# Optimization experiments

Hardware: AMD Instinct MI355X
Metric: run time of the kernel (lower is better)

Reference implementation:

```python
import jax, jax.numpy as jnp
import numpy as np

B, S, ENC, DEC, ATTN = 64, 2048, 512, 512, 256

def setup_inputs() -> dict:
    key = jax.random.key(0)
    k1, k2, k3, k4, k5 = jax.random.split(key, 5)
    s = 0.05
    return {
        "enc_outputs": jax.random.normal(k1, (B, S, ENC), dtype=jnp.float32),
        "dec_state": jax.random.normal(k2, (B, DEC), dtype=jnp.float32),
        "W_enc": jax.random.normal(k3, (ENC, ATTN), dtype=jnp.float32) * s,
        "W_dec": jax.random.normal(k4, (DEC, ATTN), dtype=jnp.float32) * s,
        "v": jax.random.normal(k5, (ATTN,), dtype=jnp.float32) * s,
    }

def reference(enc_outputs, dec_state, W_enc, W_dec, v):
    # enc_proj: [B,S,A], dec_proj: [B,1,A]
    enc_proj = jnp.einsum('bse,ea->bsa', enc_outputs, W_enc)
    dec_proj = jnp.einsum('bd,da->ba', dec_state, W_dec)[:, None, :]
    scores = jnp.einsum('bsa,a->bs', jnp.tanh(enc_proj + dec_proj), v)  # [B,S]
    attn_weights = jax.nn.softmax(scores, axis=-1)
    context = jnp.einsum('bs,bse->be', attn_weights, enc_outputs)  # [B,ENC]
    return (context, attn_weights)
```

## Files before the change

kernel.cpp:

```cpp
#include <hip/hip_runtime.h>
#include <hip/hip_bf16.h>
#include <stdint.h>

#define B_    64
#define S_    2048
#define ENC_  512
#define ATTN_ 256

typedef __bf16 bf16;
typedef bf16  bf16x8 __attribute__((ext_vector_type(8)));
typedef float f32x4  __attribute__((ext_vector_type(4)));

__device__ __forceinline__ float fexp2(float x) {
#if __has_builtin(__builtin_amdgcn_exp2f)
    return __builtin_amdgcn_exp2f(x);
#else
    return exp2f(x);
#endif
}
__device__ __forceinline__ float frcp(float x) {
#if __has_builtin(__builtin_amdgcn_rcpf)
    return __builtin_amdgcn_rcpf(x);
#else
    return 1.0f / x;
#endif
}
__device__ __forceinline__ float fast_tanh(float x) {
    float e = fexp2(x * 2.8853900817779268f);
    return 1.0f - 2.0f * frcp(e + 1.0f);
}

__device__ __forceinline__ void async_copy16(const void* g, void* l) {
#if __has_builtin(__builtin_amdgcn_global_load_lds)
    __builtin_amdgcn_global_load_lds(
        (__attribute__((address_space(1))) void*)(g),
        (__attribute__((address_space(3))) void*)(l), 16, 0, 0);
#else
    *(uint4*)l = *(const uint4*)g;
#endif
}

__global__ __launch_bounds__(256) void k_prep(const float* __restrict__ W_enc,
                                              bf16* __restrict__ WT) {
    int idx = blockIdx.x * 256 + threadIdx.x;
    int n = idx >> 9;
    int k = idx & 511;
    WT[idx] = (bf16)W_enc[k * ATTN_ + n];
}

__global__ __launch_bounds__(256) void k_decproj(const float* __restrict__ dec_state,
                                                 const float* __restrict__ W_dec,
                                                 float* __restrict__ dp) {
    int b = blockIdx.x;
    int a = threadIdx.x;
    const float* ds = dec_state + b * 512;
    float acc = 0.f;
#pragma unroll 8
    for (int d = 0; d < 512; ++d)
        acc += ds[d] * W_dec[d * ATTN_ + a];
    dp[b * ATTN_ + a] = acc;
}

__global__ __launch_bounds__(256) void k_scores(
    const float* __restrict__ enc,
    const bf16*  __restrict__ WT,
    const float* __restrict__ dp,
    const float* __restrict__ v,
    float* __restrict__ out_scores)
{
    __shared__ __align__(16) bf16 As[64 * 32];
    __shared__ __align__(16) bf16 Bs[256 * 32];
    __shared__ float partial[4][32];

    const int tid  = threadIdx.x;
    const int wave = tid >> 6;
    const int lane = tid & 63;
    const int m0   = blockIdx.x * 64;
    const int b    = m0 >> 11;

    const int mrow0 = (wave >> 1) * 32;
    const int ncol0 = (wave & 1) * 128;
    const int l15 = lane & 15;
    const int q   = lane >> 4;

    float dpv[8], vv[8];
#pragma unroll
    for (int nt = 0; nt < 8; ++nt) {
        int col = ncol0 + nt * 16 + l15;
        dpv[nt] = dp[b * 256 + col];
        vv[nt]  = v[col];
    }

    const f32x4 zero4 = {0.f, 0.f, 0.f, 0.f};
    f32x4 acc[2][8];
#pragma unroll
    for (int mt = 0; mt < 2; ++mt)
#pragma unroll
        for (int nt = 0; nt < 8; ++nt)
            acc[mt][nt] = zero4;

    const int arow = tid >> 2;
    const int ac   = tid & 3;
    const int aphys = ac ^ ((arow >> 1) & 3);
    const float* ag = enc + (size_t)(m0 + arow) * 512 + ac * 8;

    const int bn4 = tid >> 2;
    const int bc  = tid & 3;

    for (int ks = 0; ks < 16; ++ks) {
        float4 f0 = *(const float4*)(ag + ks * 32);
        float4 f1 = *(const float4*)(ag + ks * 32 + 4);
        bf16x8 av;
        av[0]=(bf16)f0.x; av[1]=(bf16)f0.y; av[2]=(bf16)f0.z; av[3]=(bf16)f0.w;
        av[4]=(bf16)f1.x; av[5]=(bf16)f1.y; av[6]=(bf16)f1.z; av[7]=(bf16)f1.w;
        *(bf16x8*)(&As[arow * 32 + aphys * 8]) = av;

#pragma unroll
        for (int r = 0; r < 4; ++r) {
            int n = r * 64 + bn4;
            int c = bc ^ ((n >> 1) & 3);
            const bf16* src = WT + (size_t)n * 512 + ks * 32 + c * 8;
            async_copy16(src, &Bs[r * 2048 + tid * 8]);
        }
        __syncthreads();

        bf16x8 af[2];
#pragma unroll
        for (int mt = 0; mt < 2; ++mt) {
            int row = mrow0 + mt * 16 + l15;
            int p = q ^ ((row >> 1) & 3);
            af[mt] = *(const bf16x8*)(&As[row * 32 + p * 8]);
        }
#pragma unroll
        for (int nt = 0; nt < 8; ++nt) {
            int n = ncol0 + nt * 16 + l15;
            int p = q ^ ((n >> 1) & 3);
            bf16x8 bfr = *(const bf16x8*)(&Bs[n * 32 + p * 8]);
            acc[0][nt] = __builtin_amdgcn_mfma_f32_16x16x32_bf16(af[0], bfr, acc[0][nt], 0, 0, 0);
            acc[1][nt] = __builtin_amdgcn_mfma_f32_16x16x32_bf16(af[1], bfr, acc[1][nt], 0, 0, 0);
        }
        __syncthreads();
    }

    float ps[2][4];
#pragma unroll
    for (int mt = 0; mt < 2; ++mt)
#pragma unroll
        for (int r = 0; r < 4; ++r) {
            float s = 0.f;
#pragma unroll
            for (int nt = 0; nt < 8; ++nt)
                s += fast_tanh(acc[mt][nt][r] + dpv[nt]) * vv[nt];
            s += __shfl_xor(s, 1, 16);
            s += __shfl_xor(s, 2, 16);
            s += __shfl_xor(s, 4, 16);
            s += __shfl_xor(s, 8, 16);
            ps[mt][r] = s;
        }
    if (l15 == 0) {
#pragma unroll
        for (int mt = 0; mt < 2; ++mt)
#pragma unroll
            for (int r = 0; r < 4; ++r)
                partial[wave][mt * 16 + q * 4 + r] = ps[mt][r];
    }
    __syncthreads();
    if (tid < 64) {
        int half = tid >> 5;
        int rr = tid & 31;
        out_scores[m0 + tid] = partial[half * 2][rr] + partial[half * 2 + 1][rr];
    }
}

__global__ __launch_bounds__(256) void k_softmax(float* __restrict__ attn) {
    int b = blockIdx.x;
    float* s = attn + b * 2048;
    __shared__ float red[256];
    int tid = threadIdx.x;

    float x[8];
    float mx = -1e30f;
#pragma unroll
    for (int i = 0; i < 8; ++i) { x[i] = s[tid + 256 * i]; mx = fmaxf(mx, x[i]); }
    red[tid] = mx;
    __syncthreads();
    for (int off = 128; off > 0; off >>= 1) {
        if (tid < off) red[tid] = fmaxf(red[tid], red[tid + off]);
        __syncthreads();
    }
    mx = red[0];
    __syncthreads();

    float e[8];
    float lsum = 0.f;
#pragma unroll
    for (int i = 0; i < 8; ++i) { e[i] = fexp2((x[i] - mx) * 1.4426950408889634f); lsum += e[i]; }
    red[tid] = lsum;
    __syncthreads();
    for (int off = 128; off > 0; off >>= 1) {
        if (tid < off) red[tid] += red[tid + off];
        __syncthreads();
    }
    float inv = 1.0f / red[0];
#pragma unroll
    for (int i = 0; i < 8; ++i) s[tid + 256 * i] = e[i] * inv;
}

__global__ __launch_bounds__(256) void k_context(const float* __restrict__ enc,
                                                 const float* __restrict__ attn,
                                                 float* __restrict__ ctx) {
    int b     = blockIdx.x >> 4;
    int chunk = blockIdx.x & 15;
    int tid = threadIdx.x;
    int e  = chunk * 32 + (tid & 31);
    int sg = tid >> 5;
    const float* eb = enc + (size_t)b * 2048 * 512;
    const float* w  = attn + b * 2048;
    float acc = 0.f;
#pragma unroll 8
    for (int s = 2047 - sg; s >= 0; s -= 8)
        acc += w[s] * eb[(size_t)s * 512 + e];
    __shared__ float red[256];
    red[tid] = acc;
    __syncthreads();
    if (tid < 32) {
        float t = red[tid] + red[tid + 32] + red[tid + 64] + red[tid + 96]
                + red[tid + 128] + red[tid + 160] + red[tid + 192] + red[tid + 224];
        ctx[b * 512 + chunk * 32 + tid] = t;
    }
}

extern "C" void kernel_launch(void* const* d_in, const int* in_sizes, int n_in,
                              void* d_out, int out_size, void* d_ws, size_t ws_size,
                              hipStream_t stream) {
    const float* enc       = (const float*)d_in[0];
    const float* dec_state = (const float*)d_in[1];
    const float* W_enc     = (const float*)d_in[2];
    const float* W_dec     = (const float*)d_in[3];
    const float* v         = (const float*)d_in[4];

    float* ctx  = (float*)d_out;
    float* attn = (float*)d_out + 64 * 512;

    char* ws = (char*)d_ws;
    bf16*  WT = (bf16*)ws;
    float* dp = (float*)(ws + 256 * 512 * sizeof(bf16));

    k_prep   <<<512, 256, 0, stream>>>(W_enc, WT);
    k_decproj<<<64, 256, 0, stream>>>(dec_state, W_dec, dp);
    k_scores <<<2048, 256, 0, stream>>>(enc, WT, dp, v, attn);
    k_softmax<<<64, 256, 0, stream>>>(attn);
    k_context<<<1024, 256, 0, stream>>>(enc, attn, ctx);
}
```

Measured before the change: 459.1 us.

## Drop LDS staging in scores GEMM, widen wave tiles, split context reduction

The scores kernel no longer stages tiles through LDS. Each wave now loads its own A rows directly into registers, with a one-step prefetch, and reads W^T fragments straight from global memory/L2. Each wave covers 32 rows by all 256 columns, so no cross-wave reduction and no barriers are needed, and occupancy is hinted at 2. The prep and decproj kernels are merged into one launch, and the context kernel is replaced by float4-vectorized slab partials plus a small reduction kernel. The tradeoffs are more register pressure and repeated global reads of W^T by every wave, in exchange for no LDS traffic and no synchronization.

```diff
diff --git a/kernel.cpp b/kernel.cpp
--- a/kernel.cpp
+++ b/kernel.cpp
@@ -30,145 +30,114 @@
     return 1.0f - 2.0f * frcp(e + 1.0f);
 }
 
-__device__ __forceinline__ void async_copy16(const void* g, void* l) {
-#if __has_builtin(__builtin_amdgcn_global_load_lds)
-    __builtin_amdgcn_global_load_lds(
-        (__attribute__((address_space(1))) void*)(g),
-        (__attribute__((address_space(3))) void*)(l), 16, 0, 0);
-#else
-    *(uint4*)l = *(const uint4*)g;
-#endif
-}
-
-__global__ __launch_bounds__(256) void k_prep(const float* __restrict__ W_enc,
-                                              bf16* __restrict__ WT) {
-    int idx = blockIdx.x * 256 + threadIdx.x;
-    int n = idx >> 9;
-    int k = idx & 511;
-    WT[idx] = (bf16)W_enc[k * ATTN_ + n];
-}
-
-__global__ __launch_bounds__(256) void k_decproj(const float* __restrict__ dec_state,
-                                                 const float* __restrict__ W_dec,
-                                                 float* __restrict__ dp) {
-    int b = blockIdx.x;
-    int a = threadIdx.x;
-    const float* ds = dec_state + b * 512;
-    float acc = 0.f;
+__global__ __launch_bounds__(256) void k_setup(const float* __restrict__ W_enc,
+                                               const float* __restrict__ dec_state,
+                                               const float* __restrict__ W_dec,
+                                               bf16* __restrict__ WT,
+                                               float* __restrict__ dp) {
+    int blk = blockIdx.x;
+    if (blk < 512) {
+        int idx = blk * 256 + threadIdx.x;
+        int n = idx >> 9;
+        int k = idx & 511;
+        WT[idx] = (bf16)W_enc[k * ATTN_ + n];
+    } else {
+        int b = blk - 512;
+        int a = threadIdx.x;
+        const float* ds = dec_state + b * 512;
+        float acc = 0.f;
 #pragma unroll 8
-    for (int d = 0; d < 512; ++d)
-        acc += ds[d] * W_dec[d * ATTN_ + a];
-    dp[b * ATTN_ + a] = acc;
-}
-
-__global__ __launch_bounds__(256) void k_scores(
+        for (int d = 0; d < 512; ++d)
+            acc += ds[d] * W_dec[d * ATTN_ + a];
+        dp[b * ATTN_ + a] = acc;
+    }
+}
+
+__global__ __launch_bounds__(256, 2) void k_scores(
     const float* __restrict__ enc,
     const bf16*  __restrict__ WT,
     const float* __restrict__ dp,
     const float* __restrict__ v,
     float* __restrict__ out_scores)
 {
-    __shared__ __align__(16) bf16 As[64 * 32];
-    __shared__ __align__(16) bf16 Bs[256 * 32];
-    __shared__ float partial[4][32];
-
     const int tid  = threadIdx.x;
     const int wave = tid >> 6;
     const int lane = tid & 63;
-    const int m0   = blockIdx.x * 64;
-    const int b    = m0 >> 11;
-
-    const int mrow0 = (wave >> 1) * 32;
-    const int ncol0 = (wave & 1) * 128;
-    const int l15 = lane & 15;
-    const int q   = lane >> 4;
-
-    float dpv[8], vv[8];
-#pragma unroll
-    for (int nt = 0; nt < 8; ++nt) {
-        int col = ncol0 + nt * 16 + l15;
+    const int l15  = lane & 15;
+    const int q    = lane >> 4;
+    const int row0 = blockIdx.x * 128 + wave * 32;
+    const int b    = row0 >> 11;
+
+    const f32x4 zero4 = {0.f, 0.f, 0.f, 0.f};
+    f32x4 acc[2][16];
+#pragma unroll
+    for (int mt = 0; mt < 2; ++mt)
+#pragma unroll
+        for (int nt = 0; nt < 16; ++nt)
+            acc[mt][nt] = zero4;
+
+    const float* ag0 = enc + (size_t)(row0 + l15) * 512 + q * 8;
+    const float* ag1 = ag0 + 16 * 512;
+    const bf16*  bg  = WT + (size_t)l15 * 512 + q * 8;
+
+    float4 a0 = *(const float4*)(ag0);
+    float4 a1 = *(const float4*)(ag0 + 4);
+    float4 a2 = *(const float4*)(ag1);
+    float4 a3 = *(const float4*)(ag1 + 4);
+
+    for (int ks = 0; ks < 16; ++ks) {
+        int ksn = (ks < 15) ? (ks + 1) : 15;
+        float4 n0 = *(const float4*)(ag0 + ksn * 32);
+        float4 n1 = *(const float4*)(ag0 + ksn * 32 + 4);
+        float4 n2 = *(const float4*)(ag1 + ksn * 32);
+        float4 n3 = *(const float4*)(ag1 + ksn * 32 + 4);
+
+        bf16x8 af0, af1;
+        af0[0]=(bf16)a0.x; af0[1]=(bf16)a0.y; af0[2]=(bf16)a0.z; af0[3]=(bf16)a0.w;
+        af0[4]=(bf16)a1.x; af0[5]=(bf16)a1.y; af0[6]=(bf16)a1.z; af0[7]=(bf16)a1.w;
+        af1[0]=(bf16)a2.x; af1[1]=(bf16)a2.y; af1[2]=(bf16)a2.z; af1[3]=(bf16)a2.w;
+        af1[4]=(bf16)a3.x; af1[5]=(bf16)a3.y; af1[6]=(bf16)a3.z; af1[7]=(bf16)a3.w;
+
+#pragma unroll
+        for (int h = 0; h < 2; ++h) {
+            bf16x8 bfr[8];
+#pragma unroll
+            for (int j = 0; j < 8; ++j) {
+                int nt = h * 8 + j;
+                bfr[j] = *(const bf16x8*)(bg + (size_t)nt * 16 * 512 + ks * 32);
+            }
+#pragma unroll
+            for (int j = 0; j < 8; ++j) {
+                int nt = h * 8 + j;
+                acc[0][nt] = __builtin_amdgcn_mfma_f32_16x16x32_bf16(af0, bfr[j], acc[0][nt], 0, 0, 0);
+                acc[1][nt] = __builtin_amdgcn_mfma_f32_16x16x32_bf16(af1, bfr[j], acc[1][nt], 0, 0, 0);
+            }
+        }
+        a0 = n0; a1 = n1; a2 = n2; a3 = n3;
+    }
+
+    float dpv[16], vv[16];
+#pragma unroll
+    for (int nt = 0; nt < 16; ++nt) {
+        int col = nt * 16 + l15;
         dpv[nt] = dp[b * 256 + col];
         vv[nt]  = v[col];
     }
-
-    const f32x4 zero4 = {0.f, 0.f, 0.f, 0.f};
-    f32x4 acc[2][8];
-#pragma unroll
-    for (int mt = 0; mt < 2; ++mt)
-#pragma unroll
-        for (int nt = 0; nt < 8; ++nt)
-            acc[mt][nt] = zero4;
-
-    const int arow = tid >> 2;
-    const int ac   = tid & 3;
-    const int aphys = ac ^ ((arow >> 1) & 3);
-    const float* ag = enc + (size_t)(m0 + arow) * 512 + ac * 8;
-
-    const int bn4 = tid >> 2;
-    const int bc  = tid & 3;
-
-    for (int ks = 0; ks < 16; ++ks) {
-        float4 f0 = *(const float4*)(ag + ks * 32);
-        float4 f1 = *(const float4*)(ag + ks * 32 + 4);
-        bf16x8 av;
-        av[0]=(bf16)f0.x; av[1]=(bf16)f0.y; av[2]=(bf16)f0.z; av[3]=(bf16)f0.w;
-        av[4]=(bf16)f1.x; av[5]=(bf16)f1.y; av[6]=(bf16)f1.z; av[7]=(bf16)f1.w;
-        *(bf16x8*)(&As[arow * 32 + aphys * 8]) = av;
-
-#pragma unroll
-        for (int r = 0; r < 4; ++r) {
-            int n = r * 64 + bn4;
-            int c = bc ^ ((n >> 1) & 3);
-            const bf16* src = WT + (size_t)n * 512 + ks * 32 + c * 8;
-            async_copy16(src, &Bs[r * 2048 + tid * 8]);
-        }
-        __syncthreads();
-
-        bf16x8 af[2];
-#pragma unroll
-        for (int mt = 0; mt < 2; ++mt) {
-            int row = mrow0 + mt * 16 + l15;
-            int p = q ^ ((row >> 1) & 3);
-            af[mt] = *(const bf16x8*)(&As[row * 32 + p * 8]);
-        }
-#pragma unroll
-        for (int nt = 0; nt < 8; ++nt) {
-            int n = ncol0 + nt * 16 + l15;
-            int p = q ^ ((n >> 1) & 3);
-            bf16x8 bfr = *(const bf16x8*)(&Bs[n * 32 + p * 8]);
-            acc[0][nt] = __builtin_amdgcn_mfma_f32_16x16x32_bf16(af[0], bfr, acc[0][nt], 0, 0, 0);
-            acc[1][nt] = __builtin_amdgcn_mfma_f32_16x16x32_bf16(af[1], bfr, acc[1][nt], 0, 0, 0);
-        }
-        __syncthreads();
-    }
-
-    float ps[2][4];
-#pragma unroll
-    for (int mt = 0; mt < 2; ++mt)
+#pragma unroll
+    for (int mt = 0; mt < 2; ++mt) {
 #pragma unroll
         for (int r = 0; r < 4; ++r) {
             float s = 0.f;
 #pragma unroll
-            for (int nt = 0; nt < 8; ++nt)
+            for (int nt = 0; nt < 16; ++nt)
                 s += fast_tanh(acc[mt][nt][r] + dpv[nt]) * vv[nt];
             s += __shfl_xor(s, 1, 16);
             s += __shfl_xor(s, 2, 16);
             s += __shfl_xor(s, 4, 16);
             s += __shfl_xor(s, 8, 16);
-            ps[mt][r] = s;
+            if (l15 == 0)
+                out_scores[row0 + mt * 16 + q * 4 + r] = s;
         }
-    if (l15 == 0) {
-#pragma unroll
-        for (int mt = 0; mt < 2; ++mt)
-#pragma unroll
-            for (int r = 0; r < 4; ++r)
-                partial[wave][mt * 16 + q * 4 + r] = ps[mt][r];
-    }
-    __syncthreads();
-    if (tid < 64) {
-        int half = tid >> 5;
-        int rr = tid & 31;
-        out_scores[m0 + tid] = partial[half * 2][rr] + partial[half * 2 + 1][rr];
     }
 }
 
@@ -208,26 +177,40 @@
 
 __global__ __launch_bounds__(256) void k_context(const float* __restrict__ enc,
                                                  const float* __restrict__ attn,
-                                                 float* __restrict__ ctx) {
-    int b     = blockIdx.x >> 4;
-    int chunk = blockIdx.x & 15;
-    int tid = threadIdx.x;
-    int e  = chunk * 32 + (tid & 31);
-    int sg = tid >> 5;
-    const float* eb = enc + (size_t)b * 2048 * 512;
-    const float* w  = attn + b * 2048;
-    float acc = 0.f;
-#pragma unroll 8
-    for (int s = 2047 - sg; s >= 0; s -= 8)
-        acc += w[s] * eb[(size_t)s * 512 + e];
-    __shared__ float red[256];
-    red[tid] = acc;
-    __syncthreads();
-    if (tid < 32) {
-        float t = red[tid] + red[tid + 32] + red[tid + 64] + red[tid + 96]
-                + red[tid + 128] + red[tid + 160] + red[tid + 192] + red[tid + 224];
-        ctx[b * 512 + chunk * 32 + tid] = t;
-    }
+                                                 float* __restrict__ partial) {
+    int b    = blockIdx.x >> 3;
+    int slab = blockIdx.x & 7;
+    int tid  = threadIdx.x;
+    int eq   = tid & 127;
+    int sr   = tid >> 7;
+    const float* eb = enc + ((size_t)b * 2048 + slab * 256) * 512;
+    const float* w  = attn + b * 2048 + slab * 256;
+
+    f32x4 acc = {0.f, 0.f, 0.f, 0.f};
+#pragma unroll 4
+    for (int s = sr; s < 256; s += 2) {
+        float ws = w[s];
+        f32x4 ev = *(const f32x4*)(eb + (size_t)s * 512 + eq * 4);
+        acc += ev * ws;
+    }
+    __shared__ f32x4 red[128];
+    if (sr) red[eq] = acc;
+    __syncthreads();
+    if (!sr) {
+        acc += red[eq];
+        *(f32x4*)(partial + (size_t)blockIdx.x * 512 + eq * 4) = acc;
+    }
+}
+
+__global__ __launch_bounds__(128) void k_ctxred(const float* __restrict__ partial,
+                                                float* __restrict__ ctx) {
+    int b  = blockIdx.x;
+    int eq = threadIdx.x;
+    f32x4 a = {0.f, 0.f, 0.f, 0.f};
+#pragma unroll
+    for (int slab = 0; slab < 8; ++slab)
+        a += *(const f32x4*)(partial + ((size_t)b * 8 + slab) * 512 + eq * 4);
+    *(f32x4*)(ctx + b * 512 + eq * 4) = a;
 }
 
 extern "C" void kernel_launch(void* const* d_in, const int* in_sizes, int n_in,
@@ -242,13 +225,14 @@
     float* ctx  = (float*)d_out;
     float* attn = (float*)d_out + 64 * 512;
 
-    char* ws = (char*)d_ws;
-    bf16*  WT = (bf16*)ws;
-    float* dp = (float*)(ws + 256 * 512 * sizeof(bf16));
-
-    k_prep   <<<512, 256, 0, stream>>>(W_enc, WT);
-    k_decproj<<<64, 256, 0, stream>>>(dec_state, W_dec, dp);
-    k_scores <<<2048, 256, 0, stream>>>(enc, WT, dp, v, attn);
+    char*  ws      = (char*)d_ws;
+    bf16*  WT      = (bf16*)ws;
+    float* dp      = (float*)(ws + 256 * 1024);
+    float* partial = (float*)(ws + 256 * 1024 + 64 * 1024);
+
+    k_setup  <<<576, 256, 0, stream>>>(W_enc, dec_state, W_dec, WT, dp);
+    k_scores <<<1024, 256, 0, stream>>>(enc, WT, dp, v, attn);
     k_softmax<<<64, 256, 0, stream>>>(attn);
-    k_context<<<1024, 256, 0, stream>>>(enc, attn, ctx);
-}
+    k_context<<<512, 256, 0, stream>>>(enc, attn, partial);
+    k_ctxred <<<64, 128, 0, stream>>>(partial, ctx);
+}
```

Measured after the change: 523.6 us. +14.1%, slower.
